# Performance work log

Measured on AMD Instinct MI355X. Metric: run time of the kernel, lower is better.

## Reference

```python
import jax, jax.numpy as jnp
import numpy as np

B, N, D, NS, ITERS = 32, 2048, 512, 8, 3
EPS = 1e-8
SCALE = D ** -0.5
LN_EPS = 1e-5


def _ln(x, g, b):
    m = x.mean(-1, keepdims=True)
    v = ((x - m) ** 2).mean(-1, keepdims=True)
    return (x - m) * jax.lax.rsqrt(v + LN_EPS) * g + b


def setup_inputs() -> dict:
    key = jax.random.key(0)
    ks = iter(jax.random.split(key, 40))
    w = lambda *s: jax.random.normal(next(ks), s, jnp.float32) * 0.02
    inp = {
        'inputs': jax.random.normal(next(ks), (B, N, D), jnp.float32),
        'slot_noise': jax.random.normal(next(ks), (B, NS, D), jnp.float32),
        'slots_mu': jax.random.normal(next(ks), (1, 1, D), jnp.float32),
        'slots_logsigma': w(1, 1, D),
        'k_w': w(D, D), 'k_b': jnp.zeros((D,), jnp.float32),
        'v_w': w(D, D), 'v_b': jnp.zeros((D,), jnp.float32),
        'gru_w_ih': w(3 * D, D), 'gru_w_hh': w(3 * D, D),
        'gru_b_ih': jnp.zeros((3 * D,), jnp.float32),
        'gru_b_hh': jnp.zeros((3 * D,), jnp.float32),
        'ln_in_g': jnp.ones((D,), jnp.float32), 'ln_in_b': jnp.zeros((D,), jnp.float32),
        'ln_slots_g': jnp.ones((D,), jnp.float32), 'ln_slots_b': jnp.zeros((D,), jnp.float32),
        'ln_pre_g': jnp.ones((D,), jnp.float32), 'ln_pre_b': jnp.zeros((D,), jnp.float32),
        'mlp1_w': w(1024, D), 'mlp1_b': jnp.zeros((1024,), jnp.float32),
        'mlp2_w': w(1024, 1024), 'mlp2_b': jnp.zeros((1024,), jnp.float32),
        'mlp3_w': w(512, 1024), 'mlp3_b': jnp.zeros((512,), jnp.float32),
        'mlp4_w': w(256, 512), 'mlp4_b': jnp.zeros((256,), jnp.float32),
    }
    return inp


def reference(inputs, slot_noise, slots_mu, slots_logsigma, k_w, k_b, v_w, v_b,
              gru_w_ih, gru_w_hh, gru_b_ih, gru_b_hh,
              ln_in_g, ln_in_b, ln_slots_g, ln_slots_b, ln_pre_g, ln_pre_b,
              mlp1_w, mlp1_b, mlp2_w, mlp2_b, mlp3_w, mlp3_b, mlp4_w, mlp4_b):
    b, n, d = inputs.shape
    # stochastic slot init: mu + exp(logsigma) * noise  -> [b, ns, d]
    slots = slots_mu + jnp.exp(slots_logsigma) * slot_noise
    x = _ln(inputs, ln_in_g, ln_in_b)
    k = x @ k_w.T + k_b
    v = x @ v_w.T + v_b
    updates = slots
    for _ in range(ITERS):
        slots_prev = slots
        q = _ln(slots, ln_slots_g, ln_slots_b)
        dots = jnp.einsum('bid,bjd->bij', q, k) * SCALE  # [b, ns, n]
        attn = jax.nn.softmax(dots, axis=1) + EPS        # softmax over slot axis
        attn = attn / attn.sum(-1, keepdims=True)        # renorm over tokens
        updates = jnp.einsum('bjd,bij->bid', v, attn)    # [b, ns, d]
        # GRUCell(updates, slots_prev), then residual add of updates
        u = updates.reshape(-1, d)
        h = slots_prev.reshape(-1, d)
        gi = u @ gru_w_ih.T + gru_b_ih
        gh = h @ gru_w_hh.T + gru_b_hh
        i_r, i_z, i_n = jnp.split(gi, 3, axis=-1)
        h_r, h_z, h_n = jnp.split(gh, 3, axis=-1)
        r = jax.nn.sigmoid(i_r + h_r)
        z = jax.nn.sigmoid(i_z + h_z)
        nn_ = jnp.tanh(i_n + r * h_n)
        h_new = (1.0 - z) * nn_ + z * h
        slots = (u + h_new).reshape(b, -1, d)
    # output MLP with exact GELU (torch default)
    s = _ln(slots, ln_pre_g, ln_pre_b)
    s = jax.nn.gelu(s @ mlp1_w.T + mlp1_b, approximate=False)
    s = jax.nn.gelu(s @ mlp2_w.T + mlp2_b, approximate=False)
    s = jax.nn.gelu(s @ mlp3_w.T + mlp3_b, approximate=False)
    s = s @ mlp4_w.T + mlp4_b
    return (updates, s)
```

## Files before the change

### kernel.cpp

```cpp
#include <hip/hip_runtime.h>
#include <math.h>

#define Bb 32
#define Nn 2048
#define Dd 512
#define NS 8
#define ITERS 3
#define EPSf 1e-8f
#define SCALEf 0.04419417382415922f
#define LN_EPSf 1e-5f

#define QHS 520
#define PTS 136
#define CHUNKS 16

typedef _Float16 half8 __attribute__((ext_vector_type(8)));
typedef float f32x4 __attribute__((ext_vector_type(4)));

__device__ __forceinline__ float waveReduceSum(float v) {
    #pragma unroll
    for (int m = 32; m >= 1; m >>= 1) v += __shfl_xor(v, m);
    return v;
}

__device__ __forceinline__ float gelu_exact(float x) {
    return 0.5f * x * (1.0f + erff(x * 0.7071067811865476f));
}

__device__ __forceinline__ void async_copy16(const _Float16* g, _Float16* l) {
    __builtin_amdgcn_global_load_lds(
        (const __attribute__((address_space(1))) unsigned int*)g,
        (__attribute__((address_space(3))) unsigned int*)l, 16, 0, 0);
}

__global__ __launch_bounds__(256) void megapack_kernel(
    const float* __restrict__ k_w, const float* __restrict__ v_w,
    const float* __restrict__ w_ih, const float* __restrict__ w_hh,
    const float* __restrict__ m1, const float* __restrict__ m2,
    const float* __restrict__ m3, const float* __restrict__ m4,
    _Float16* __restrict__ Bkv, _Float16* __restrict__ Bih, _Float16* __restrict__ Bhh,
    _Float16* __restrict__ Bm1, _Float16* __restrict__ Bm2,
    _Float16* __restrict__ Bm3, _Float16* __restrict__ Bm4) {
    int bid = blockIdx.x, tid = threadIdx.x;
    const float* src; _Float16* dst; int kbits, base;
    if (bid < 2048) {
        int i = bid * 256 + tid;
        Bkv[i] = (_Float16)(i < 262144 ? k_w[i] : v_w[i - 262144]);
        return;
    }
    else if (bid < 5120)  { src = w_ih; dst = Bih; kbits = 9;  base = 2048; }
    else if (bid < 8192)  { src = w_hh; dst = Bhh; kbits = 9;  base = 5120; }
    else if (bid < 10240) { src = m1;   dst = Bm1; kbits = 9;  base = 8192; }
    else if (bid < 14336) { src = m2;   dst = Bm2; kbits = 10; base = 10240; }
    else if (bid < 16384) { src = m3;   dst = Bm3; kbits = 10; base = 14336; }
    else                  { src = m4;   dst = Bm4; kbits = 9;  base = 16384; }
    int e = (bid - base) * 256 + tid;
    int K = 1 << kbits;
    int row = e >> kbits, k = e & (K - 1);
    _Float16 h = (_Float16)src[e];
    _Float16* d = dst + ((size_t)row << (kbits + 1));
    d[k] = h;
    d[K + k] = h;
}

__global__ __launch_bounds__(256) void pack_ln_single_kernel(
    const float* __restrict__ x, const float* __restrict__ g, const float* __restrict__ b,
    _Float16* __restrict__ Ap) {
    int wid = blockIdx.x * 4 + (threadIdx.x >> 6);
    int lane = threadIdx.x & 63;
    const float4* row4 = (const float4*)(x + (size_t)wid * Dd);
    float4 va = row4[lane * 2], vb = row4[lane * 2 + 1];
    float v[8] = {va.x, va.y, va.z, va.w, vb.x, vb.y, vb.z, vb.w};
    float s = 0.f, sq = 0.f;
    #pragma unroll
    for (int t = 0; t < 8; ++t) { s += v[t]; sq += v[t] * v[t]; }
    s = waveReduceSum(s);
    sq = waveReduceSum(sq);
    float m = s * (1.0f / Dd);
    float var = sq * (1.0f / Dd) - m * m;
    float rs = rsqrtf(var + LN_EPSf);
    const float4* g4 = (const float4*)g;
    const float4* b4 = (const float4*)b;
    float4 ga = g4[lane * 2], gb = g4[lane * 2 + 1];
    float4 ba = b4[lane * 2], bb = b4[lane * 2 + 1];
    float gg[8] = {ga.x, ga.y, ga.z, ga.w, gb.x, gb.y, gb.z, gb.w};
    float bbv[8] = {ba.x, ba.y, ba.z, ba.w, bb.x, bb.y, bb.z, bb.w};
    half8 o;
    #pragma unroll
    for (int t = 0; t < 8; ++t) o[t] = (_Float16)((v[t] - m) * rs * gg[t] + bbv[t]);
    *(half8*)(Ap + (size_t)wid * Dd + lane * 8) = o;
}

__global__ __launch_bounds__(256) void slots_init_kernel(
    const float* __restrict__ noise, const float* __restrict__ mu,
    const float* __restrict__ ls, float* __restrict__ slots, _Float16* __restrict__ A2,
    const float* __restrict__ lns_g, const float* __restrict__ lns_b,
    _Float16* __restrict__ qh) {
    int row = blockIdx.x * 4 + (threadIdx.x >> 6);
    int lane = threadIdx.x & 63;
    float val[8];
    float s = 0.f, sq = 0.f;
    #pragma unroll
    for (int t = 0; t < 8; ++t) {
        int d = t * 64 + lane;
        float v = mu[d] + expf(ls[d]) * noise[(size_t)row * 512 + d];
        val[t] = v;
        s += v; sq += v * v;
        slots[(size_t)row * 512 + d] = v;
        _Float16 hi = (_Float16)v;
        A2[(size_t)(256 + row) * 1024 + d] = hi;
        A2[(size_t)(256 + row) * 1024 + 512 + d] = (_Float16)(v - (float)hi);
    }
    s = waveReduceSum(s);
    sq = waveReduceSum(sq);
    float m = s * (1.0f / Dd);
    float var = sq * (1.0f / Dd) - m * m;
    float rs = rsqrtf(var + LN_EPSf);
    #pragma unroll
    for (int t = 0; t < 8; ++t) {
        int d = t * 64 + lane;
        qh[(size_t)row * 512 + d] = (_Float16)(((val[t] - m) * rs * lns_g[d] + lns_b[d]) * SCALEf);
    }
}

__global__ __launch_bounds__(256) void kv_hgemm_kernel(
    const _Float16* __restrict__ Apack, const _Float16* __restrict__ Bkv,
    const float* __restrict__ k_b, const float* __restrict__ v_b,
    _Float16* __restrict__ khalf, _Float16* __restrict__ vT) {
    __shared__ _Float16 smem[17408];
    _Float16* As = smem;
    _Float16* Bs = smem + 8192;
    const int f = blockIdx.x;
    const int m0 = ((f & 7) + ((f >> 6) << 3)) * 128;
    const int n0 = ((f >> 3) & 7) * 128;
    const int tid = threadIdx.x;
    const int w = tid >> 6, lane = tid & 63;
    const int r8 = lane >> 3, seg = lane & 7;
    const int lr = lane & 15, quad = lane >> 4;
    const int wm = w >> 1, wn = w & 1;
    f32x4 acc[4][4];
    #pragma unroll
    for (int i = 0; i < 4; ++i)
        #pragma unroll
        for (int j = 0; j < 4; ++j) acc[i][j] = (f32x4){0.f, 0.f, 0.f, 0.f};
    for (int k0 = 0; k0 < 512; k0 += 64) {
        __syncthreads();
        #pragma unroll
        for (int g = 0; g < 4; ++g) {
            int grp = w * 4 + g;
            int row = grp * 8 + r8;
            async_copy16(Apack + (size_t)(m0 + row) * 512 + k0 + seg * 8, As + grp * 512);
            async_copy16(Bkv + (size_t)(n0 + row) * 512 + k0 + seg * 8, Bs + grp * 512);
        }
        __syncthreads();
        #pragma unroll
        for (int kk = 0; kk < 2; ++kk) {
            half8 a[4], b[4];
            #pragma unroll
            for (int t = 0; t < 4; ++t) {
                a[t] = *(const half8*)(As + (wm * 64 + t * 16 + lr) * 64 + kk * 32 + quad * 8);
                b[t] = *(const half8*)(Bs + (wn * 64 + t * 16 + lr) * 64 + kk * 32 + quad * 8);
            }
            #pragma unroll
            for (int mt = 0; mt < 4; ++mt)
                #pragma unroll
                for (int nt = 0; nt < 4; ++nt)
                    acc[mt][nt] = __builtin_amdgcn_mfma_f32_16x16x32_f16(
                        a[mt], b[nt], acc[mt][nt], 0, 0, 0);
        }
    }
    __syncthreads();
    const bool isK = (n0 < 512);
    #pragma unroll
    for (int mt = 0; mt < 4; ++mt)
        #pragma unroll
        for (int nt = 0; nt < 4; ++nt) {
            int ml = wm * 64 + mt * 16 + quad * 4;
            int nl = wn * 64 + nt * 16 + lr;
            float bv = isK ? k_b[n0 + nl] : v_b[n0 - 512 + nl];
            #pragma unroll
            for (int r = 0; r < 4; ++r) {
                _Float16 h = (_Float16)(acc[mt][nt][r] + bv);
                if (isK) smem[(ml + r) * 136 + nl] = h;
                else     smem[nl * 136 + ml + r] = h;
            }
        }
    __syncthreads();
    int r = tid >> 1, half = tid & 1;
    _Float16* dst;
    if (isK) {
        dst = khalf + (size_t)(m0 + r) * 512 + n0 + half * 64;
    } else {
        int b = m0 >> 11, j0 = m0 & 2047, d0 = n0 - 512;
        dst = vT + ((size_t)b * 512 + d0 + r) * 2048 + j0 + half * 64;
    }
    #pragma unroll
    for (int c = 0; c < 8; ++c)
        *(half8*)(dst + c * 8) = *(const half8*)(smem + r * 136 + half * 64 + c * 8);
}

__global__ __launch_bounds__(256) void attn_kernel(
    const _Float16* __restrict__ qh_g,
    const _Float16* __restrict__ khalf, const _Float16* __restrict__ vT,
    float* __restrict__ rawp, float* __restrict__ sumsp) {
    const int b = blockIdx.y, chunk = blockIdx.x;
    __shared__ _Float16 qh[16 * QHS];
    __shared__ _Float16 pT[16 * PTS];
    __shared__ float sums_lds[64];
    const int tid = threadIdx.x, w = tid >> 6, lane = tid & 63;
    const int lr = lane & 15, quad = lane >> 4;

    {
        int r = tid >> 5;
        int c = (tid & 31) * 16;
        *(half8*)(qh + r * QHS + c) = *(const half8*)(qh_g + ((size_t)b * NS + r) * 512 + c);
        *(half8*)(qh + r * QHS + c + 8) = *(const half8*)(qh_g + ((size_t)b * NS + r) * 512 + c + 8);
        half8 z = {};
        *(half8*)(qh + (8 + r) * QHS + c) = z;
        *(half8*)(qh + (8 + r) * QHS + c + 8) = z;
    }
    __syncthreads();

    const int j0 = chunk * 128 + w * 32;
    f32x4 dots[2];
    dots[0] = (f32x4){0.f, 0.f, 0.f, 0.f};
    dots[1] = (f32x4){0.f, 0.f, 0.f, 0.f};
    for (int ks = 0; ks < 16; ++ks) {
        half8 bq = *(const half8*)(qh + lr * QHS + ks * 32 + quad * 8);
        #pragma unroll
        for (int mf = 0; mf < 2; ++mf) {
            half8 ak = *(const half8*)(khalf + ((size_t)b * Nn + j0 + mf * 16 + lr) * 512 + ks * 32 + quad * 8);
            dots[mf] = __builtin_amdgcn_mfma_f32_16x16x32_f16(ak, bq, dots[mf], 0, 0, 0);
        }
    }
    float ssum = 0.f;
    #pragma unroll
    for (int mf = 0; mf < 2; ++mf) {
        f32x4 d = dots[mf];
        f32x4 mx = d;
        #pragma unroll
        for (int msk = 1; msk <= 4; msk <<= 1) {
            #pragma unroll
            for (int r = 0; r < 4; ++r) mx[r] = fmaxf(mx[r], __shfl_xor(mx[r], msk));
        }
        f32x4 p;
        #pragma unroll
        for (int r = 0; r < 4; ++r) p[r] = __expf(d[r] - mx[r]);
        f32x4 sm = p;
        #pragma unroll
        for (int msk = 1; msk <= 4; msk <<= 1) {
            #pragma unroll
            for (int r = 0; r < 4; ++r) sm[r] += __shfl_xor(sm[r], msk);
        }
        #pragma unroll
        for (int r = 0; r < 4; ++r) {
            _Float16 ph = (_Float16)(p[r] / sm[r] + EPSf);
            pT[lr * PTS + w * 32 + mf * 16 + quad * 4 + r] = ph;
            ssum += (float)ph;
        }
    }
    ssum += __shfl_xor(ssum, 16);
    ssum += __shfl_xor(ssum, 32);
    if (lane < 16) sums_lds[w * 16 + lane] = ssum;
    __syncthreads();

    f32x4 acc[8];
    #pragma unroll
    for (int nf = 0; nf < 8; ++nf) acc[nf] = (f32x4){0.f, 0.f, 0.f, 0.f};
    #pragma unroll
    for (int kc = 0; kc < 4; ++kc) {
        half8 ap = *(const half8*)(pT + lr * PTS + kc * 32 + quad * 8);
        #pragma unroll
        for (int nf = 0; nf < 8; ++nf) {
            int dcol = w * 128 + nf * 16 + lr;
            half8 bv = *(const half8*)(vT + ((size_t)b * 512 + dcol) * 2048 + chunk * 128 + kc * 32 + quad * 8);
            acc[nf] = __builtin_amdgcn_mfma_f32_16x16x32_f16(ap, bv, acc[nf], 0, 0, 0);
        }
    }
    if (quad < 2) {
        #pragma unroll
        for (int nf = 0; nf < 8; ++nf) {
            #pragma unroll
            for (int r = 0; r < 4; ++r) {
                int slot = quad * 4 + r;
                rawp[(((size_t)chunk * Bb + b) * NS + slot) * Dd + w * 128 + nf * 16 + lr] = acc[nf][r];
            }
        }
    }
    if (w == 0 && lane < NS) {
        float tot = sums_lds[lane] + sums_lds[16 + lane] + sums_lds[32 + lane] + sums_lds[48 + lane];
        sumsp[((size_t)chunk * Bb + b) * NS + lane] = tot;
    }
}

__global__ __launch_bounds__(256) void finalize_kernel(
    const float* __restrict__ rawp, const float* __restrict__ sumsp,
    float* __restrict__ u, float* __restrict__ out0, _Float16* __restrict__ A2) {
    int idx = blockIdx.x * 256 + threadIdx.x;
    int row = idx >> 9, k = idx & 511;
    float rs = 0.f, ss = 0.f;
    #pragma unroll
    for (int c = 0; c < CHUNKS; ++c) {
        rs += rawp[(size_t)c * 131072 + idx];
        ss += sumsp[c * 256 + row];
    }
    float val = rs / ss;
    u[idx] = val;
    out0[idx] = val;
    _Float16 hi = (_Float16)val;
    A2[(size_t)row * 1024 + k] = hi;
    A2[(size_t)row * 1024 + 512 + k] = (_Float16)(val - (float)hi);
}

__device__ __forceinline__ void hgemm64_core(
    const _Float16* __restrict__ A, const _Float16* __restrict__ Bw,
    int K2, f32x4 acc[2][2], _Float16* As, _Float16* Bs) {
    const int tid = threadIdx.x;
    const int w = tid >> 6, lane = tid & 63;
    const int r8 = lane >> 3, seg = lane & 7;
    const int lr = lane & 15, quad = lane >> 4;
    const int wm = w >> 1, wn = w & 1;
    for (int k0 = 0; k0 < K2; k0 += 64) {
        __syncthreads();
        #pragma unroll
        for (int p = 0; p < 2; ++p) {
            int grp = p * 4 + w;
            int row = grp * 8 + r8;
            async_copy16(A + (size_t)row * K2 + k0 + seg * 8, As + grp * 512);
            async_copy16(Bw + (size_t)row * K2 + k0 + seg * 8, Bs + grp * 512);
        }
        __syncthreads();
        #pragma unroll
        for (int kk = 0; kk < 2; ++kk) {
            half8 a[2], b[2];
            #pragma unroll
            for (int t = 0; t < 2; ++t) {
                a[t] = *(const half8*)(As + (wm * 32 + t * 16 + lr) * 64 + kk * 32 + quad * 8);
                b[t] = *(const half8*)(Bs + (wn * 32 + t * 16 + lr) * 64 + kk * 32 + quad * 8);
            }
            #pragma unroll
            for (int mt = 0; mt < 2; ++mt)
                #pragma unroll
                for (int nt = 0; nt < 2; ++nt)
                    acc[mt][nt] = __builtin_amdgcn_mfma_f32_16x16x32_f16(
                        a[mt], b[nt], acc[mt][nt], 0, 0, 0);
        }
    }
}

template <int ACT, int PACK>
__global__ __launch_bounds__(256) void hgemm64_kernel(
    const _Float16* __restrict__ A, const _Float16* __restrict__ Bw,
    const float* __restrict__ bias, float* __restrict__ C, _Float16* __restrict__ P,
    int K2, int N, int Kp) {
    __shared__ _Float16 As[4096], Bs[4096];
    const int m0 = blockIdx.y * 64, n0 = blockIdx.x * 64;
    f32x4 acc[2][2];
    #pragma unroll
    for (int i = 0; i < 2; ++i)
        #pragma unroll
        for (int j = 0; j < 2; ++j) acc[i][j] = (f32x4){0.f, 0.f, 0.f, 0.f};
    hgemm64_core(A + (size_t)m0 * K2, Bw + (size_t)n0 * K2, K2, acc, As, Bs);
    const int tid = threadIdx.x;
    const int w = tid >> 6, lane = tid & 63;
    const int lr = lane & 15, quad = lane >> 4;
    const int wm = w >> 1, wn = w & 1;
    #pragma unroll
    for (int mt = 0; mt < 2; ++mt)
        #pragma unroll
        for (int nt = 0; nt < 2; ++nt) {
            int n = n0 + wn * 32 + nt * 16 + lr;
            float bv = bias[n];
            #pragma unroll
            for (int r = 0; r < 4; ++r) {
                int m = m0 + wm * 32 + mt * 16 + quad * 4 + r;
                float val = acc[mt][nt][r] + bv;
                if (ACT) val = gelu_exact(val);
                if (PACK) {
                    _Float16 hi = (_Float16)val;
                    P[(size_t)m * 2 * Kp + n] = hi;
                    P[(size_t)m * 2 * Kp + Kp + n] = (_Float16)(val - (float)hi);
                } else {
                    C[(size_t)m * N + n] = val;
                }
            }
        }
}

__global__ __launch_bounds__(256) void gru_gemm_kernel(
    const _Float16* __restrict__ A2, const _Float16* __restrict__ Bih,
    const _Float16* __restrict__ Bhh, const float* __restrict__ b_ih,
    const float* __restrict__ b_hh, float* __restrict__ gi, float* __restrict__ gh) {
    __shared__ _Float16 As[4096], Bs[4096];
    const int by = blockIdx.y;
    const int n0 = blockIdx.x * 64;
    const _Float16* Ap; const _Float16* Bw; const float* bias; float* C;
    if (by < 4) { Ap = A2 + (size_t)by * 64 * 1024;        Bw = Bih; bias = b_ih; C = gi + (size_t)by * 64 * 1536; }
    else        { Ap = A2 + (size_t)(256 + (by - 4) * 64) * 1024; Bw = Bhh; bias = b_hh; C = gh + (size_t)(by - 4) * 64 * 1536; }
    f32x4 acc[2][2];
    #pragma unroll
    for (int i = 0; i < 2; ++i)
        #pragma unroll
        for (int j = 0; j < 2; ++j) acc[i][j] = (f32x4){0.f, 0.f, 0.f, 0.f};
    hgemm64_core(Ap, Bw + (size_t)n0 * 1024, 1024, acc, As, Bs);
    const int tid = threadIdx.x;
    const int w = tid >> 6, lane = tid & 63;
    const int lr = lane & 15, quad = lane >> 4;
    const int wm = w >> 1, wn = w & 1;
    #pragma unroll
    for (int mt = 0; mt < 2; ++mt)
        #pragma unroll
        for (int nt = 0; nt < 2; ++nt) {
            int n = n0 + wn * 32 + nt * 16 + lr;
            float bv = bias[n];
            #pragma unroll
            for (int r = 0; r < 4; ++r) {
                int m = wm * 32 + mt * 16 + quad * 4 + r;
                C[(size_t)m * 1536 + n] = acc[mt][nt][r] + bv;
            }
        }
}

__global__ __launch_bounds__(256) void gru_elem_kernel(
    const float* __restrict__ gi, const float* __restrict__ gh,
    const float* __restrict__ u, float* __restrict__ slots, _Float16* __restrict__ A2,
    const float* __restrict__ lns_g, const float* __restrict__ lns_b,
    _Float16* __restrict__ qh,
    const float* __restrict__ lnp_g, const float* __restrict__ lnp_b,
    _Float16* __restrict__ P1, int last) {
    int row = blockIdx.x * 4 + (threadIdx.x >> 6);
    int lane = threadIdx.x & 63;
    const float* gir = gi + (size_t)row * 1536;
    const float* ghr = gh + (size_t)row * 1536;
    float val[8];
    #pragma unroll
    for (int t = 0; t < 8; ++t) {
        int d = t * 64 + lane;
        float ir = gir[d], iz = gir[512 + d], in_ = gir[1024 + d];
        float hr = ghr[d], hz = ghr[512 + d], hn = ghr[1024 + d];
        float r = 1.0f / (1.0f + expf(-(ir + hr)));
        float z = 1.0f / (1.0f + expf(-(iz + hz)));
        float n = tanhf(in_ + r * hn);
        float h = slots[(size_t)row * 512 + d];
        float hnew = (1.0f - z) * n + z * h;
        float vv = u[(size_t)row * 512 + d] + hnew;
        val[t] = vv;
        slots[(size_t)row * 512 + d] = vv;
        _Float16 hi = (_Float16)vv;
        A2[(size_t)(256 + row) * 1024 + d] = hi;
        A2[(size_t)(256 + row) * 1024 + 512 + d] = (_Float16)(vv - (float)hi);
    }
    float s = 0.f, sq = 0.f;
    #pragma unroll
    for (int t = 0; t < 8; ++t) { s += val[t]; sq += val[t] * val[t]; }
    s = waveReduceSum(s);
    sq = waveReduceSum(sq);
    float m = s * (1.0f / Dd);
    float var = sq * (1.0f / Dd) - m * m;
    float rs = rsqrtf(var + LN_EPSf);
    if (!last) {
        #pragma unroll
        for (int t = 0; t < 8; ++t) {
            int d = t * 64 + lane;
            qh[(size_t)row * 512 + d] =
                (_Float16)(((val[t] - m) * rs * lns_g[d] + lns_b[d]) * SCALEf);
        }
    } else {
        #pragma unroll
        for (int t = 0; t < 8; ++t) {
            int d = t * 64 + lane;
            float a = (val[t] - m) * rs * lnp_g[d] + lnp_b[d];
            _Float16 hi = (_Float16)a;
            P1[(size_t)row * 1024 + d] = hi;
            P1[(size_t)row * 1024 + 512 + d] = (_Float16)(a - (float)hi);
        }
    }
}

extern "C" void kernel_launch(void* const* d_in, const int* in_sizes, int n_in,
                              void* d_out, int out_size, void* d_ws, size_t ws_size,
                              hipStream_t stream) {
    const float* inputs   = (const float*)d_in[0];
    const float* noise    = (const float*)d_in[1];
    const float* mu       = (const float*)d_in[2];
    const float* lsig     = (const float*)d_in[3];
    const float* k_w      = (const float*)d_in[4];
    const float* k_b      = (const float*)d_in[5];
    const float* v_w      = (const float*)d_in[6];
    const float* v_b      = (const float*)d_in[7];
    const float* w_ih     = (const float*)d_in[8];
    const float* w_hh     = (const float*)d_in[9];
    const float* b_ih     = (const float*)d_in[10];
    const float* b_hh     = (const float*)d_in[11];
    const float* ln_in_g  = (const float*)d_in[12];
    const float* ln_in_b  = (const float*)d_in[13];
    const float* ln_s_g   = (const float*)d_in[14];
    const float* ln_s_b   = (const float*)d_in[15];
    const float* ln_p_g   = (const float*)d_in[16];
    const float* ln_p_b   = (const float*)d_in[17];
    const float* mlp1_w   = (const float*)d_in[18];
    const float* mlp1_b   = (const float*)d_in[19];
    const float* mlp2_w   = (const float*)d_in[20];
    const float* mlp2_b   = (const float*)d_in[21];
    const float* mlp3_w   = (const float*)d_in[22];
    const float* mlp3_b   = (const float*)d_in[23];
    const float* mlp4_w   = (const float*)d_in[24];
    const float* mlp4_b   = (const float*)d_in[25];
    float* out0 = (float*)d_out;
    float* out1 = (float*)d_out + Bb * NS * Dd;

    char* wp = (char*)d_ws;
    auto alloc = [&](size_t bytes) -> void* {
        void* p = (void*)wp;
        wp += (bytes + 255) & ~(size_t)255;
        return p;
    };
    const size_t MR = (size_t)Bb * Nn;
    _Float16* Apack = (_Float16*)alloc(MR * 512 * 2);
    _Float16* khalf = (_Float16*)alloc(MR * 512 * 2);
    _Float16* vT    = (_Float16*)alloc((size_t)Bb * 512 * Nn * 2);
    _Float16* Bkv   = (_Float16*)alloc((size_t)1024 * 512 * 2);
    _Float16* Bih   = (_Float16*)alloc((size_t)1536 * 1024 * 2);
    _Float16* Bhh   = (_Float16*)alloc((size_t)1536 * 1024 * 2);
    _Float16* Bm1   = (_Float16*)alloc((size_t)1024 * 1024 * 2);
    _Float16* Bm2   = (_Float16*)alloc((size_t)1024 * 2048 * 2);
    _Float16* Bm3   = (_Float16*)alloc((size_t)512 * 2048 * 2);
    _Float16* Bm4   = (_Float16*)alloc((size_t)256 * 1024 * 2);
    float* slots    = (float*)alloc((size_t)Bb * NS * Dd * 4);
    _Float16* qh    = (_Float16*)alloc((size_t)Bb * NS * Dd * 2);
    float* rawp     = (float*)alloc((size_t)CHUNKS * Bb * NS * Dd * 4);
    float* sumsp    = (float*)alloc((size_t)CHUNKS * Bb * NS * 4);
    float* ubuf     = (float*)alloc((size_t)Bb * NS * Dd * 4);
    float* gi       = (float*)alloc((size_t)Bb * NS * 1536 * 4);
    float* gh       = (float*)alloc((size_t)Bb * NS * 1536 * 4);
    _Float16* A2    = (_Float16*)alloc((size_t)512 * 1024 * 2);
    _Float16* P1    = (_Float16*)alloc((size_t)256 * 1024 * 2);
    _Float16* P2    = (_Float16*)alloc((size_t)256 * 2048 * 2);
    _Float16* P3    = (_Float16*)alloc((size_t)256 * 2048 * 2);
    _Float16* P4    = (_Float16*)alloc((size_t)256 * 1024 * 2);

    megapack_kernel<<<16896, 256, 0, stream>>>(
        k_w, v_w, w_ih, w_hh, mlp1_w, mlp2_w, mlp3_w, mlp4_w,
        Bkv, Bih, Bhh, Bm1, Bm2, Bm3, Bm4);
    pack_ln_single_kernel<<<MR / 4, 256, 0, stream>>>(inputs, ln_in_g, ln_in_b, Apack);
    slots_init_kernel<<<64, 256, 0, stream>>>(noise, mu, lsig, slots, A2, ln_s_g, ln_s_b, qh);

    kv_hgemm_kernel<<<4096, 256, 0, stream>>>(Apack, Bkv, k_b, v_b, khalf, vT);

    for (int it = 0; it < ITERS; ++it) {
        attn_kernel<<<dim3(CHUNKS, Bb), 256, 0, stream>>>(qh, khalf, vT, rawp, sumsp);
        finalize_kernel<<<512, 256, 0, stream>>>(rawp, sumsp, ubuf, out0, A2);
        gru_gemm_kernel<<<dim3(24, 8), 256, 0, stream>>>(A2, Bih, Bhh, b_ih, b_hh, gi, gh);
        gru_elem_kernel<<<64, 256, 0, stream>>>(gi, gh, ubuf, slots, A2,
                                                ln_s_g, ln_s_b, qh,
                                                ln_p_g, ln_p_b, P1, it == ITERS - 1 ? 1 : 0);
    }

    hgemm64_kernel<1, 1><<<dim3(16, 4), 256, 0, stream>>>(P1, Bm1, mlp1_b, nullptr, P2, 1024, 1024, 1024);
    hgemm64_kernel<1, 1><<<dim3(16, 4), 256, 0, stream>>>(P2, Bm2, mlp2_b, nullptr, P3, 2048, 1024, 1024);
    hgemm64_kernel<1, 1><<<dim3(8, 4), 256, 0, stream>>>(P3, Bm3, mlp3_b, nullptr, P4, 2048, 512, 512);
    hgemm64_kernel<0, 0><<<dim3(4, 4), 256, 0, stream>>>(P4, Bm4, mlp4_b, out1, nullptr, 1024, 256, 256);
}
```

Before: 656.8 us.

## Fold K/V projections into queries and outputs, skip materializing K and V

Removes the large K/V GEMM over all tokens. Dots are computed as x·(q·Wk) plus a bias term q·k_b, and updates as (attn·x)·Wv^T plus v_b, so attention reads the layer-normed inputs directly. Per-iteration small GEMMs project q through Wk and the weighted token sums through Wv. The attention kernel is restructured with double-buffered async staging of input tiles. The trade-off is extra small kernels per iteration and a scalar FMA loop for the attn·x accumulation.

```diff
diff --git a/kernel.cpp b/kernel.cpp
--- a/kernel.cpp
+++ b/kernel.cpp
@@ -10,11 +10,11 @@
 #define SCALEf 0.04419417382415922f
 #define LN_EPSf 1e-5f
 
-#define QHS 520
-#define PTS 136
 #define CHUNKS 16
+#define SUBT 32
 
 typedef _Float16 half8 __attribute__((ext_vector_type(8)));
+typedef _Float16 half2v __attribute__((ext_vector_type(2)));
 typedef float f32x4 __attribute__((ext_vector_type(4)));
 
 __device__ __forceinline__ float waveReduceSum(float v) {
@@ -34,26 +34,23 @@
 }
 
 __global__ __launch_bounds__(256) void megapack_kernel(
-    const float* __restrict__ k_w, const float* __restrict__ v_w,
     const float* __restrict__ w_ih, const float* __restrict__ w_hh,
     const float* __restrict__ m1, const float* __restrict__ m2,
     const float* __restrict__ m3, const float* __restrict__ m4,
-    _Float16* __restrict__ Bkv, _Float16* __restrict__ Bih, _Float16* __restrict__ Bhh,
+    const float* __restrict__ v_w,
+    _Float16* __restrict__ Bih, _Float16* __restrict__ Bhh,
     _Float16* __restrict__ Bm1, _Float16* __restrict__ Bm2,
-    _Float16* __restrict__ Bm3, _Float16* __restrict__ Bm4) {
+    _Float16* __restrict__ Bm3, _Float16* __restrict__ Bm4,
+    _Float16* __restrict__ Bvd) {
     int bid = blockIdx.x, tid = threadIdx.x;
     const float* src; _Float16* dst; int kbits, base;
-    if (bid < 2048) {
-        int i = bid * 256 + tid;
-        Bkv[i] = (_Float16)(i < 262144 ? k_w[i] : v_w[i - 262144]);
-        return;
-    }
-    else if (bid < 5120)  { src = w_ih; dst = Bih; kbits = 9;  base = 2048; }
-    else if (bid < 8192)  { src = w_hh; dst = Bhh; kbits = 9;  base = 5120; }
-    else if (bid < 10240) { src = m1;   dst = Bm1; kbits = 9;  base = 8192; }
-    else if (bid < 14336) { src = m2;   dst = Bm2; kbits = 10; base = 10240; }
-    else if (bid < 16384) { src = m3;   dst = Bm3; kbits = 10; base = 14336; }
-    else                  { src = m4;   dst = Bm4; kbits = 9;  base = 16384; }
+    if      (bid < 3072)  { src = w_ih; dst = Bih; kbits = 9;  base = 0; }
+    else if (bid < 6144)  { src = w_hh; dst = Bhh; kbits = 9;  base = 3072; }
+    else if (bid < 8192)  { src = m1;   dst = Bm1; kbits = 9;  base = 6144; }
+    else if (bid < 12288) { src = m2;   dst = Bm2; kbits = 10; base = 8192; }
+    else if (bid < 14336) { src = m3;   dst = Bm3; kbits = 10; base = 12288; }
+    else if (bid < 14848) { src = m4;   dst = Bm4; kbits = 9;  base = 14336; }
+    else                  { src = v_w;  dst = Bvd; kbits = 9;  base = 14848; }
     int e = (bid - base) * 256 + tid;
     int K = 1 << kbits;
     int row = e >> kbits, k = e & (K - 1);
@@ -61,6 +58,26 @@
     _Float16* d = dst + ((size_t)row << (kbits + 1));
     d[k] = h;
     d[K + k] = h;
+}
+
+__global__ __launch_bounds__(256) void kwt_kernel(
+    const float* __restrict__ kw, _Float16* __restrict__ BkT) {
+    __shared__ float t[64][65];
+    const int bf = blockIdx.x * 64, bd = blockIdx.y * 64;
+    const int tid = threadIdx.x;
+    #pragma unroll
+    for (int i = 0; i < 16; ++i) {
+        int idx = i * 256 + tid;
+        int r = idx >> 6, c = idx & 63;
+        t[r][c] = kw[(size_t)(bf + r) * 512 + bd + c];
+    }
+    __syncthreads();
+    #pragma unroll
+    for (int i = 0; i < 16; ++i) {
+        int idx = i * 256 + tid;
+        int r = idx >> 6, c = idx & 63;
+        BkT[(size_t)(bd + r) * 512 + bf + c] = (_Float16)t[c][r];
+    }
 }
 
 __global__ __launch_bounds__(256) void pack_ln_single_kernel(
@@ -95,7 +112,7 @@
     const float* __restrict__ noise, const float* __restrict__ mu,
     const float* __restrict__ ls, float* __restrict__ slots, _Float16* __restrict__ A2,
     const float* __restrict__ lns_g, const float* __restrict__ lns_b,
-    _Float16* __restrict__ qh) {
+    _Float16* __restrict__ qh, const float* __restrict__ k_b, float* __restrict__ cvec) {
     int row = blockIdx.x * 4 + (threadIdx.x >> 6);
     int lane = threadIdx.x & 63;
     float val[8];
@@ -116,188 +133,134 @@
     float m = s * (1.0f / Dd);
     float var = sq * (1.0f / Dd) - m * m;
     float rs = rsqrtf(var + LN_EPSf);
+    float c = 0.f;
     #pragma unroll
     for (int t = 0; t < 8; ++t) {
         int d = t * 64 + lane;
-        qh[(size_t)row * 512 + d] = (_Float16)(((val[t] - m) * rs * lns_g[d] + lns_b[d]) * SCALEf);
-    }
-}
-
-__global__ __launch_bounds__(256) void kv_hgemm_kernel(
-    const _Float16* __restrict__ Apack, const _Float16* __restrict__ Bkv,
-    const float* __restrict__ k_b, const float* __restrict__ v_b,
-    _Float16* __restrict__ khalf, _Float16* __restrict__ vT) {
-    __shared__ _Float16 smem[17408];
-    _Float16* As = smem;
-    _Float16* Bs = smem + 8192;
-    const int f = blockIdx.x;
-    const int m0 = ((f & 7) + ((f >> 6) << 3)) * 128;
-    const int n0 = ((f >> 3) & 7) * 128;
-    const int tid = threadIdx.x;
-    const int w = tid >> 6, lane = tid & 63;
-    const int r8 = lane >> 3, seg = lane & 7;
-    const int lr = lane & 15, quad = lane >> 4;
-    const int wm = w >> 1, wn = w & 1;
-    f32x4 acc[4][4];
-    #pragma unroll
-    for (int i = 0; i < 4; ++i)
-        #pragma unroll
-        for (int j = 0; j < 4; ++j) acc[i][j] = (f32x4){0.f, 0.f, 0.f, 0.f};
-    for (int k0 = 0; k0 < 512; k0 += 64) {
-        __syncthreads();
-        #pragma unroll
-        for (int g = 0; g < 4; ++g) {
-            int grp = w * 4 + g;
-            int row = grp * 8 + r8;
-            async_copy16(Apack + (size_t)(m0 + row) * 512 + k0 + seg * 8, As + grp * 512);
-            async_copy16(Bkv + (size_t)(n0 + row) * 512 + k0 + seg * 8, Bs + grp * 512);
-        }
-        __syncthreads();
-        #pragma unroll
-        for (int kk = 0; kk < 2; ++kk) {
-            half8 a[4], b[4];
-            #pragma unroll
-            for (int t = 0; t < 4; ++t) {
-                a[t] = *(const half8*)(As + (wm * 64 + t * 16 + lr) * 64 + kk * 32 + quad * 8);
-                b[t] = *(const half8*)(Bs + (wn * 64 + t * 16 + lr) * 64 + kk * 32 + quad * 8);
-            }
-            #pragma unroll
-            for (int mt = 0; mt < 4; ++mt)
-                #pragma unroll
-                for (int nt = 0; nt < 4; ++nt)
-                    acc[mt][nt] = __builtin_amdgcn_mfma_f32_16x16x32_f16(
-                        a[mt], b[nt], acc[mt][nt], 0, 0, 0);
-        }
-    }
-    __syncthreads();
-    const bool isK = (n0 < 512);
-    #pragma unroll
-    for (int mt = 0; mt < 4; ++mt)
-        #pragma unroll
-        for (int nt = 0; nt < 4; ++nt) {
-            int ml = wm * 64 + mt * 16 + quad * 4;
-            int nl = wn * 64 + nt * 16 + lr;
-            float bv = isK ? k_b[n0 + nl] : v_b[n0 - 512 + nl];
-            #pragma unroll
-            for (int r = 0; r < 4; ++r) {
-                _Float16 h = (_Float16)(acc[mt][nt][r] + bv);
-                if (isK) smem[(ml + r) * 136 + nl] = h;
-                else     smem[nl * 136 + ml + r] = h;
-            }
-        }
-    __syncthreads();
-    int r = tid >> 1, half = tid & 1;
-    _Float16* dst;
-    if (isK) {
-        dst = khalf + (size_t)(m0 + r) * 512 + n0 + half * 64;
-    } else {
-        int b = m0 >> 11, j0 = m0 & 2047, d0 = n0 - 512;
-        dst = vT + ((size_t)b * 512 + d0 + r) * 2048 + j0 + half * 64;
-    }
-    #pragma unroll
-    for (int c = 0; c < 8; ++c)
-        *(half8*)(dst + c * 8) = *(const half8*)(smem + r * 136 + half * 64 + c * 8);
+        float qv = ((val[t] - m) * rs * lns_g[d] + lns_b[d]) * SCALEf;
+        qh[(size_t)row * 512 + d] = (_Float16)qv;
+        c += qv * k_b[d];
+    }
+    c = waveReduceSum(c);
+    if (lane == 0) cvec[row] = c;
 }
 
 __global__ __launch_bounds__(256) void attn_kernel(
-    const _Float16* __restrict__ qh_g,
-    const _Float16* __restrict__ khalf, const _Float16* __restrict__ vT,
+    const _Float16* __restrict__ Apack, const _Float16* __restrict__ Qk,
+    const float* __restrict__ cvec,
     float* __restrict__ rawp, float* __restrict__ sumsp) {
     const int b = blockIdx.y, chunk = blockIdx.x;
-    __shared__ _Float16 qh[16 * QHS];
-    __shared__ _Float16 pT[16 * PTS];
-    __shared__ float sums_lds[64];
+    __shared__ _Float16 Xs[2][SUBT * 512];
+    __shared__ _Float16 aTh[SUBT][8];
+    __shared__ float dlo[SUBT][8];
+    __shared__ float sred[2][8];
     const int tid = threadIdx.x, w = tid >> 6, lane = tid & 63;
     const int lr = lane & 15, quad = lane >> 4;
-
-    {
-        int r = tid >> 5;
-        int c = (tid & 31) * 16;
-        *(half8*)(qh + r * QHS + c) = *(const half8*)(qh_g + ((size_t)b * NS + r) * 512 + c);
-        *(half8*)(qh + r * QHS + c + 8) = *(const half8*)(qh_g + ((size_t)b * NS + r) * 512 + c + 8);
-        half8 z = {};
-        *(half8*)(qh + (8 + r) * QHS + c) = z;
-        *(half8*)(qh + (8 + r) * QHS + c + 8) = z;
-    }
+    const int mt = w & 1, hl = w >> 1;
+    const size_t tokbase = (size_t)b * Nn + chunk * 128;
+
+    const float cv = cvec[b * 8 + (lr & 7)];
+    const _Float16* qkrow = Qk + ((size_t)(b * 8 + (lr & 7)) << 10) + hl * 512;
+
+    float2 w8[8];
+    #pragma unroll
+    for (int s = 0; s < 8; ++s) w8[s] = (float2){0.f, 0.f};
+    float ssum_part = 0.f;
+    const int d0 = w * 128 + lane * 2;
+    const int pvslot = d0 >> 3, pvsub = d0 & 7;
+
+    auto STAGE = [&](int st, int buf) {
+        #pragma unroll
+        for (int i = 0; i < 8; ++i) {
+            int row = i * 4 + w;
+            const _Float16* src = Apack + (tokbase + st * SUBT + row) * 512 +
+                                  ((lane ^ (row & 7)) << 3);
+            async_copy16(src, &Xs[buf][row * 512]);
+        }
+    };
+
+    STAGE(0, 0);
+    for (int st = 0; st < 4; ++st) {
+        const int cur = st & 1;
+        STAGE(st < 3 ? st + 1 : 3, cur ^ 1);
+        asm volatile("s_waitcnt vmcnt(8)" ::: "memory");
+        __syncthreads();
+        const _Float16* Xc = &Xs[cur][0];
+        f32x4 dots = (f32x4){0.f, 0.f, 0.f, 0.f};
+        const int rr = mt * 16 + lr;
+        #pragma unroll
+        for (int ks = 0; ks < 16; ++ks) {
+            half8 ax = *(const half8*)(Xc + rr * 512 +
+                       ((((ks << 2) | quad) ^ (rr & 7)) << 3));
+            half8 bq = *(const half8*)(qkrow + ks * 32 + quad * 8);
+            dots = __builtin_amdgcn_mfma_f32_16x16x32_f16(ax, bq, dots, 0, 0, 0);
+        }
+        if (hl == 1 && lr < 8) {
+            #pragma unroll
+            for (int r = 0; r < 4; ++r) dlo[mt * 16 + quad * 4 + r][lr] = dots[r];
+        }
+        __syncthreads();
+        if (hl == 0) {
+            f32x4 d;
+            #pragma unroll
+            for (int r = 0; r < 4; ++r)
+                d[r] = dots[r] + dlo[mt * 16 + quad * 4 + r][lr & 7] + cv;
+            f32x4 mx = d;
+            #pragma unroll
+            for (int msk = 1; msk <= 4; msk <<= 1) {
+                #pragma unroll
+                for (int r = 0; r < 4; ++r) mx[r] = fmaxf(mx[r], __shfl_xor(mx[r], msk));
+            }
+            f32x4 p;
+            #pragma unroll
+            for (int r = 0; r < 4; ++r) p[r] = __expf(d[r] - mx[r]);
+            f32x4 sm = p;
+            #pragma unroll
+            for (int msk = 1; msk <= 4; msk <<= 1) {
+                #pragma unroll
+                for (int r = 0; r < 4; ++r) sm[r] += __shfl_xor(sm[r], msk);
+            }
+            #pragma unroll
+            for (int r = 0; r < 4; ++r) {
+                _Float16 ph = (_Float16)(p[r] / sm[r] + EPSf);
+                if (lr < 8) aTh[mt * 16 + quad * 4 + r][lr] = ph;
+                ssum_part += (float)ph;
+            }
+        }
+        __syncthreads();
+        #pragma unroll 4
+        for (int t = 0; t < SUBT; ++t) {
+            half8 aa = *(const half8*)&aTh[t][0];
+            half2v xv = *(const half2v*)(Xc + t * 512 +
+                        ((pvslot ^ (t & 7)) << 3) + pvsub);
+            float x0 = (float)xv[0], x1 = (float)xv[1];
+            #pragma unroll
+            for (int s = 0; s < 8; ++s) {
+                float av = (float)aa[s];
+                w8[s].x += av * x0;
+                w8[s].y += av * x1;
+            }
+        }
+        __syncthreads();
+    }
+    asm volatile("s_waitcnt vmcnt(0)" ::: "memory");
+
+    float* rp = rawp + ((size_t)chunk * Bb + b) * NS * Dd + d0;
+    #pragma unroll
+    for (int s = 0; s < 8; ++s) *(float2*)(rp + s * Dd) = w8[s];
+
+    ssum_part += __shfl_xor(ssum_part, 16);
+    ssum_part += __shfl_xor(ssum_part, 32);
+    if (hl == 0 && lane < 8) sred[w][lane] = ssum_part;
     __syncthreads();
-
-    const int j0 = chunk * 128 + w * 32;
-    f32x4 dots[2];
-    dots[0] = (f32x4){0.f, 0.f, 0.f, 0.f};
-    dots[1] = (f32x4){0.f, 0.f, 0.f, 0.f};
-    for (int ks = 0; ks < 16; ++ks) {
-        half8 bq = *(const half8*)(qh + lr * QHS + ks * 32 + quad * 8);
-        #pragma unroll
-        for (int mf = 0; mf < 2; ++mf) {
-            half8 ak = *(const half8*)(khalf + ((size_t)b * Nn + j0 + mf * 16 + lr) * 512 + ks * 32 + quad * 8);
-            dots[mf] = __builtin_amdgcn_mfma_f32_16x16x32_f16(ak, bq, dots[mf], 0, 0, 0);
-        }
-    }
-    float ssum = 0.f;
-    #pragma unroll
-    for (int mf = 0; mf < 2; ++mf) {
-        f32x4 d = dots[mf];
-        f32x4 mx = d;
-        #pragma unroll
-        for (int msk = 1; msk <= 4; msk <<= 1) {
-            #pragma unroll
-            for (int r = 0; r < 4; ++r) mx[r] = fmaxf(mx[r], __shfl_xor(mx[r], msk));
-        }
-        f32x4 p;
-        #pragma unroll
-        for (int r = 0; r < 4; ++r) p[r] = __expf(d[r] - mx[r]);
-        f32x4 sm = p;
-        #pragma unroll
-        for (int msk = 1; msk <= 4; msk <<= 1) {
-            #pragma unroll
-            for (int r = 0; r < 4; ++r) sm[r] += __shfl_xor(sm[r], msk);
-        }
-        #pragma unroll
-        for (int r = 0; r < 4; ++r) {
-            _Float16 ph = (_Float16)(p[r] / sm[r] + EPSf);
-            pT[lr * PTS + w * 32 + mf * 16 + quad * 4 + r] = ph;
-            ssum += (float)ph;
-        }
-    }
-    ssum += __shfl_xor(ssum, 16);
-    ssum += __shfl_xor(ssum, 32);
-    if (lane < 16) sums_lds[w * 16 + lane] = ssum;
-    __syncthreads();
-
-    f32x4 acc[8];
-    #pragma unroll
-    for (int nf = 0; nf < 8; ++nf) acc[nf] = (f32x4){0.f, 0.f, 0.f, 0.f};
-    #pragma unroll
-    for (int kc = 0; kc < 4; ++kc) {
-        half8 ap = *(const half8*)(pT + lr * PTS + kc * 32 + quad * 8);
-        #pragma unroll
-        for (int nf = 0; nf < 8; ++nf) {
-            int dcol = w * 128 + nf * 16 + lr;
-            half8 bv = *(const half8*)(vT + ((size_t)b * 512 + dcol) * 2048 + chunk * 128 + kc * 32 + quad * 8);
-            acc[nf] = __builtin_amdgcn_mfma_f32_16x16x32_f16(ap, bv, acc[nf], 0, 0, 0);
-        }
-    }
-    if (quad < 2) {
-        #pragma unroll
-        for (int nf = 0; nf < 8; ++nf) {
-            #pragma unroll
-            for (int r = 0; r < 4; ++r) {
-                int slot = quad * 4 + r;
-                rawp[(((size_t)chunk * Bb + b) * NS + slot) * Dd + w * 128 + nf * 16 + lr] = acc[nf][r];
-            }
-        }
-    }
-    if (w == 0 && lane < NS) {
-        float tot = sums_lds[lane] + sums_lds[16 + lane] + sums_lds[32 + lane] + sums_lds[48 + lane];
-        sumsp[((size_t)chunk * Bb + b) * NS + lane] = tot;
-    }
+    if (tid < 8) sumsp[((size_t)chunk * Bb + b) * NS + tid] = sred[0][tid] + sred[1][tid];
 }
 
 __global__ __launch_bounds__(256) void finalize_kernel(
     const float* __restrict__ rawp, const float* __restrict__ sumsp,
-    float* __restrict__ u, float* __restrict__ out0, _Float16* __restrict__ A2) {
+    _Float16* __restrict__ Whl) {
     int idx = blockIdx.x * 256 + threadIdx.x;
-    int row = idx >> 9, k = idx & 511;
+    int row = idx >> 9, d = idx & 511;
     float rs = 0.f, ss = 0.f;
     #pragma unroll
     for (int c = 0; c < CHUNKS; ++c) {
@@ -305,11 +268,9 @@
         ss += sumsp[c * 256 + row];
     }
     float val = rs / ss;
-    u[idx] = val;
-    out0[idx] = val;
     _Float16 hi = (_Float16)val;
-    A2[(size_t)row * 1024 + k] = hi;
-    A2[(size_t)row * 1024 + 512 + k] = (_Float16)(val - (float)hi);
+    Whl[(size_t)row * 1024 + d] = hi;
+    Whl[(size_t)row * 1024 + 512 + d] = (_Float16)(val - (float)hi);
 }
 
 __device__ __forceinline__ void hgemm64_core(
@@ -348,7 +309,7 @@
     }
 }
 
-template <int ACT, int PACK>
+template <int ACT, int PACK, int BIAS>
 __global__ __launch_bounds__(256) void hgemm64_kernel(
     const _Float16* __restrict__ A, const _Float16* __restrict__ Bw,
     const float* __restrict__ bias, float* __restrict__ C, _Float16* __restrict__ P,
@@ -370,7 +331,7 @@
         #pragma unroll
         for (int nt = 0; nt < 2; ++nt) {
             int n = n0 + wn * 32 + nt * 16 + lr;
-            float bv = bias[n];
+            float bv = BIAS ? bias[n] : 0.f;
             #pragma unroll
             for (int r = 0; r < 4; ++r) {
                 int m = m0 + wm * 32 + mt * 16 + quad * 4 + r;
@@ -387,6 +348,41 @@
         }
 }
 
+__global__ __launch_bounds__(256) void ugemm_kernel(
+    const _Float16* __restrict__ Whl, const _Float16* __restrict__ Bvd,
+    const float* __restrict__ v_b, float* __restrict__ u, float* __restrict__ out0,
+    _Float16* __restrict__ A2) {
+    __shared__ _Float16 As[4096], Bs[4096];
+    const int m0 = blockIdx.y * 64, n0 = blockIdx.x * 64;
+    f32x4 acc[2][2];
+    #pragma unroll
+    for (int i = 0; i < 2; ++i)
+        #pragma unroll
+        for (int j = 0; j < 2; ++j) acc[i][j] = (f32x4){0.f, 0.f, 0.f, 0.f};
+    hgemm64_core(Whl + (size_t)m0 * 1024, Bvd + (size_t)n0 * 1024, 1024, acc, As, Bs);
+    const int tid = threadIdx.x;
+    const int w = tid >> 6, lane = tid & 63;
+    const int lr = lane & 15, quad = lane >> 4;
+    const int wm = w >> 1, wn = w & 1;
+    #pragma unroll
+    for (int mt = 0; mt < 2; ++mt)
+        #pragma unroll
+        for (int nt = 0; nt < 2; ++nt) {
+            int n = n0 + wn * 32 + nt * 16 + lr;
+            float bv = v_b[n];
+            #pragma unroll
+            for (int r = 0; r < 4; ++r) {
+                int m = m0 + wm * 32 + mt * 16 + quad * 4 + r;
+                float val = acc[mt][nt][r] + bv;
+                u[(size_t)m * 512 + n] = val;
+                out0[(size_t)m * 512 + n] = val;
+                _Float16 hi = (_Float16)val;
+                A2[(size_t)m * 1024 + n] = hi;
+                A2[(size_t)m * 1024 + 512 + n] = (_Float16)(val - (float)hi);
+            }
+        }
+}
+
 __global__ __launch_bounds__(256) void gru_gemm_kernel(
     const _Float16* __restrict__ A2, const _Float16* __restrict__ Bih,
     const _Float16* __restrict__ Bhh, const float* __restrict__ b_ih,
@@ -425,7 +421,7 @@
     const float* __restrict__ gi, const float* __restrict__ gh,
     const float* __restrict__ u, float* __restrict__ slots, _Float16* __restrict__ A2,
     const float* __restrict__ lns_g, const float* __restrict__ lns_b,
-    _Float16* __restrict__ qh,
+    _Float16* __restrict__ qh, const float* __restrict__ k_b, float* __restrict__ cvec,
     const float* __restrict__ lnp_g, const float* __restrict__ lnp_b,
     _Float16* __restrict__ P1, int last) {
     int row = blockIdx.x * 4 + (threadIdx.x >> 6);
@@ -459,12 +455,16 @@
     float var = sq * (1.0f / Dd) - m * m;
     float rs = rsqrtf(var + LN_EPSf);
     if (!last) {
+        float c = 0.f;
         #pragma unroll
         for (int t = 0; t < 8; ++t) {
             int d = t * 64 + lane;
-            qh[(size_t)row * 512 + d] =
-                (_Float16)(((val[t] - m) * rs * lns_g[d] + lns_b[d]) * SCALEf);
-        }
+            float qv = ((val[t] - m) * rs * lns_g[d] + lns_b[d]) * SCALEf;
+            qh[(size_t)row * 512 + d] = (_Float16)qv;
+            c += qv * k_b[d];
+        }
+        c = waveReduceSum(c);
+        if (lane == 0) cvec[row] = c;
     } else {
         #pragma unroll
         for (int t = 0; t < 8; ++t) {
@@ -517,19 +517,21 @@
     };
     const size_t MR = (size_t)Bb * Nn;
     _Float16* Apack = (_Float16*)alloc(MR * 512 * 2);
-    _Float16* khalf = (_Float16*)alloc(MR * 512 * 2);
-    _Float16* vT    = (_Float16*)alloc((size_t)Bb * 512 * Nn * 2);
-    _Float16* Bkv   = (_Float16*)alloc((size_t)1024 * 512 * 2);
     _Float16* Bih   = (_Float16*)alloc((size_t)1536 * 1024 * 2);
     _Float16* Bhh   = (_Float16*)alloc((size_t)1536 * 1024 * 2);
     _Float16* Bm1   = (_Float16*)alloc((size_t)1024 * 1024 * 2);
     _Float16* Bm2   = (_Float16*)alloc((size_t)1024 * 2048 * 2);
     _Float16* Bm3   = (_Float16*)alloc((size_t)512 * 2048 * 2);
     _Float16* Bm4   = (_Float16*)alloc((size_t)256 * 1024 * 2);
+    _Float16* Bvd   = (_Float16*)alloc((size_t)512 * 1024 * 2);
+    _Float16* BkT   = (_Float16*)alloc((size_t)512 * 512 * 2);
     float* slots    = (float*)alloc((size_t)Bb * NS * Dd * 4);
     _Float16* qh    = (_Float16*)alloc((size_t)Bb * NS * Dd * 2);
+    float* cvec     = (float*)alloc((size_t)Bb * NS * 4);
+    _Float16* Qk    = (_Float16*)alloc((size_t)256 * 1024 * 2);
     float* rawp     = (float*)alloc((size_t)CHUNKS * Bb * NS * Dd * 4);
     float* sumsp    = (float*)alloc((size_t)CHUNKS * Bb * NS * 4);
+    _Float16* Whl   = (_Float16*)alloc((size_t)256 * 1024 * 2);
     float* ubuf     = (float*)alloc((size_t)Bb * NS * Dd * 4);
     float* gi       = (float*)alloc((size_t)Bb * NS * 1536 * 4);
     float* gh       = (float*)alloc((size_t)Bb * NS * 1536 * 4);
@@ -539,25 +541,28 @@
     _Float16* P3    = (_Float16*)alloc((size_t)256 * 2048 * 2);
     _Float16* P4    = (_Float16*)alloc((size_t)256 * 1024 * 2);
 
-    megapack_kernel<<<16896, 256, 0, stream>>>(
-        k_w, v_w, w_ih, w_hh, mlp1_w, mlp2_w, mlp3_w, mlp4_w,
-        Bkv, Bih, Bhh, Bm1, Bm2, Bm3, Bm4);
+    megapack_kernel<<<15872, 256, 0, stream>>>(
+        w_ih, w_hh, mlp1_w, mlp2_w, mlp3_w, mlp4_w, v_w,
+        Bih, Bhh, Bm1, Bm2, Bm3, Bm4, Bvd);
+    kwt_kernel<<<dim3(8, 8), 256, 0, stream>>>(k_w, BkT);
     pack_ln_single_kernel<<<MR / 4, 256, 0, stream>>>(inputs, ln_in_g, ln_in_b, Apack);
-    slots_init_kernel<<<64, 256, 0, stream>>>(noise, mu, lsig, slots, A2, ln_s_g, ln_s_b, qh);
-
-    kv_hgemm_kernel<<<4096, 256, 0, stream>>>(Apack, Bkv, k_b, v_b, khalf, vT);
+    slots_init_kernel<<<64, 256, 0, stream>>>(noise, mu, lsig, slots, A2,
+                                              ln_s_g, ln_s_b, qh, k_b, cvec);
 
     for (int it = 0; it < ITERS; ++it) {
-        attn_kernel<<<dim3(CHUNKS, Bb), 256, 0, stream>>>(qh, khalf, vT, rawp, sumsp);
-        finalize_kernel<<<512, 256, 0, stream>>>(rawp, sumsp, ubuf, out0, A2);
+        hgemm64_kernel<0, 1, 0><<<dim3(8, 4), 256, 0, stream>>>(
+            qh, BkT, nullptr, nullptr, Qk, 512, 512, 512);
+        attn_kernel<<<dim3(CHUNKS, Bb), 256, 0, stream>>>(Apack, Qk, cvec, rawp, sumsp);
+        finalize_kernel<<<512, 256, 0, stream>>>(rawp, sumsp, Whl);
+        ugemm_kernel<<<dim3(8, 4), 256, 0, stream>>>(Whl, Bvd, v_b, ubuf, out0, A2);
         gru_gemm_kernel<<<dim3(24, 8), 256, 0, stream>>>(A2, Bih, Bhh, b_ih, b_hh, gi, gh);
         gru_elem_kernel<<<64, 256, 0, stream>>>(gi, gh, ubuf, slots, A2,
-                                                ln_s_g, ln_s_b, qh,
+                                                ln_s_g, ln_s_b, qh, k_b, cvec,
                                                 ln_p_g, ln_p_b, P1, it == ITERS - 1 ? 1 : 0);
     }
 
-    hgemm64_kernel<1, 1><<<dim3(16, 4), 256, 0, stream>>>(P1, Bm1, mlp1_b, nullptr, P2, 1024, 1024, 1024);
-    hgemm64_kernel<1, 1><<<dim3(16, 4), 256, 0, stream>>>(P2, Bm2, mlp2_b, nullptr, P3, 2048, 1024, 1024);
-    hgemm64_kernel<1, 1><<<dim3(8, 4), 256, 0, stream>>>(P3, Bm3, mlp3_b, nullptr, P4, 2048, 512, 512);
-    hgemm64_kernel<0, 0><<<dim3(4, 4), 256, 0, stream>>>(P4, Bm4, mlp4_b, out1, nullptr, 1024, 256, 256);
-}
+    hgemm64_kernel<1, 1, 1><<<dim3(16, 4), 256, 0, stream>>>(P1, Bm1, mlp1_b, nullptr, P2, 1024, 1024, 1024);
+    hgemm64_kernel<1, 1, 1><<<dim3(16, 4), 256, 0, stream>>>(P2, Bm2, mlp2_b, nullptr, P3, 2048, 1024, 1024);
+    hgemm64_kernel<1, 1, 1><<<dim3(8, 4), 256, 0, stream>>>(P3, Bm3, mlp3_b, nullptr, P4, 2048, 512, 512);
+    hgemm64_kernel<0, 0, 1><<<dim3(4, 4), 256, 0, stream>>>(P4, Bm4, mlp4_b, out1, nullptr, 1024, 256, 256);
+}
```

Measured after the change: 566.5 us. 13.7% less time.
